# Kernel tuning notes

Hardware: AMD Instinct MI355X
Metric: run time of the kernel (lower is better)

Reference implementation:

```python
import jax, jax.numpy as jnp
import numpy as np

T, D, E, I, TOP_K = 4096, 2048, 8, 4096, 2

def setup_inputs() -> dict:
    key = jax.random.key(0)
    k1, k2, k3, k4, k5 = jax.random.split(key, 5)
    s = 0.02
    return {
        "hidden_states": jax.random.normal(k1, (T, D), jnp.float32),
        "wr": jax.random.normal(k2, (E, D), jnp.float32) * s,
        "w1": jax.random.normal(k3, (E, I, D), jnp.float32) * s,
        "v1": jax.random.normal(k4, (E, I, D), jnp.float32) * s,
        "w2": jax.random.normal(k5, (E, D, I), jnp.float32) * s,
        "index": 0,
    }

def reference(hidden_states, wr, w1, v1, w2, index):
    # index selects the layer; n_layers == 1 here so weights are already that layer's.
    x = hidden_states.reshape(-1, D)  # [T, D]
    # Router logits + softmax top-k with renormalization (fused_moe semantics)
    logits = x @ wr.T                                  # [T, E]
    probs = jax.nn.softmax(logits, axis=-1)
    topw, topi = jax.lax.top_k(probs, TOP_K)           # [T, K]
    topw = topw / jnp.sum(topw, axis=-1, keepdims=True)
    # Dense per-token gate matrix, zero for non-selected experts
    t_idx = jnp.arange(x.shape[0])[:, None]
    gates = jnp.zeros((x.shape[0], E), x.dtype).at[t_idx, topi].set(topw)  # [T, E]
    # SiLU-GLU experts: (silu(x w1^T) * (x v1^T)) w2^T, combined by gates
    out = jnp.zeros_like(x)
    for e in range(E):  # fixed small expert count
        h = jax.nn.silu(x @ w1[e].T) * (x @ v1[e].T)   # [T, I]
        out = out + gates[:, e:e + 1] * (h @ w2[e].T)  # [T, D]
    return out
```

## Files before the change

kernel.cpp:

```cpp
#include <hip/hip_runtime.h>
#include <hip/hip_bf16.h>
#include <cstdint>


#define T_TOK 4096
#define DHID  2048
#define NEXP  8
#define IDIM  4096
#define NSLOT (T_TOK * 2)

#define BM 128
#define BK 64

typedef __bf16 bf16x8 __attribute__((ext_vector_type(8)));
typedef __bf16 bf16x4 __attribute__((ext_vector_type(4)));
typedef float  f32x4  __attribute__((ext_vector_type(4)));

__device__ __forceinline__ void gload_lds16(const void* g, void* l) {
    __builtin_amdgcn_global_load_lds(
        (const __attribute__((address_space(1))) uint32_t*)g,
        (__attribute__((address_space(3))) uint32_t*)l, 16, 0, 0);
}

__global__ __launch_bounds__(256) void router_kernel(
    const float* __restrict__ x, const float* __restrict__ wr,
    __bf16* __restrict__ xb, int* __restrict__ topi, float* __restrict__ topg,
    int* __restrict__ cnt)
{
    int wave = threadIdx.x >> 6, lane = threadIdx.x & 63;
    int t = blockIdx.x * 4 + wave;
    const float4* xr = (const float4*)(x + (size_t)t * DHID);
    bf16x4* xbo = (bf16x4*)(xb + (size_t)t * DHID);
    float acc[NEXP];
#pragma unroll
    for (int e = 0; e < NEXP; ++e) acc[e] = 0.f;
#pragma unroll
    for (int j = 0; j < DHID / 256; ++j) {
        int d4 = lane + j * 64;
        float4 v = xr[d4];
        bf16x4 bv;
        bv[0] = (__bf16)v.x; bv[1] = (__bf16)v.y;
        bv[2] = (__bf16)v.z; bv[3] = (__bf16)v.w;
        xbo[d4] = bv;
#pragma unroll
        for (int e = 0; e < NEXP; ++e) {
            float4 w = ((const float4*)(wr + e * DHID))[d4];
            acc[e] += v.x * w.x + v.y * w.y + v.z * w.z + v.w * w.w;
        }
    }
#pragma unroll
    for (int e = 0; e < NEXP; ++e) {
#pragma unroll
        for (int s = 32; s > 0; s >>= 1) acc[e] += __shfl_xor(acc[e], s);
    }
    if (lane == 0) {
        int e0 = 0; float l0 = acc[0];
#pragma unroll
        for (int e = 1; e < NEXP; ++e) if (acc[e] > l0) { l0 = acc[e]; e0 = e; }
        int e1 = -1; float l1 = -3.4e38f;
#pragma unroll
        for (int e = 0; e < NEXP; ++e) if (e != e0 && acc[e] > l1) { l1 = acc[e]; e1 = e; }
        float g0 = 1.f / (1.f + __expf(l1 - l0));
        topi[t * 2] = e0; topi[t * 2 + 1] = e1;
        topg[t * 2] = g0; topg[t * 2 + 1] = 1.f - g0;
        atomicAdd(&cnt[e0], 1); atomicAdd(&cnt[e1], 1);
    }
}

__global__ void scan_kernel(const int* __restrict__ cnt, int* __restrict__ basep,
                            int* __restrict__ fill)
{
    if (threadIdx.x == 0 && blockIdx.x == 0) {
        int s = 0;
#pragma unroll
        for (int e = 0; e < NEXP; ++e) { basep[e] = s; s += cnt[e]; fill[e] = 0; }
    }
}

__global__ __launch_bounds__(256) void assign_kernel(
    const int* __restrict__ topi, const float* __restrict__ topg,
    const int* __restrict__ basep, int* __restrict__ fill,
    int* __restrict__ tok_of_slot, float* __restrict__ gate_of_slot,
    int* __restrict__ slot_of)
{
    int t = blockIdx.x * 256 + threadIdx.x;
    if (t >= T_TOK) return;
#pragma unroll
    for (int k = 0; k < 2; ++k) {
        int e = topi[t * 2 + k];
        int slot = basep[e] + atomicAdd(&fill[e], 1);
        tok_of_slot[slot] = t;
        gate_of_slot[slot] = topg[t * 2 + k];
        slot_of[t * 2 + k] = slot;
    }
}

__global__ __launch_bounds__(256) void convert2_kernel(
    const float* __restrict__ s1, __bf16* __restrict__ d1,
    const float* __restrict__ s2, __bf16* __restrict__ d2, size_t n8)
{
    for (size_t i = (size_t)blockIdx.x * 256 + threadIdx.x; i < n8;
         i += (size_t)gridDim.x * 256) {
        {
            const float4* s = (const float4*)(s1 + i * 8);
            float4 a = s[0], b = s[1];
            bf16x8 o;
            o[0]=(__bf16)a.x; o[1]=(__bf16)a.y; o[2]=(__bf16)a.z; o[3]=(__bf16)a.w;
            o[4]=(__bf16)b.x; o[5]=(__bf16)b.y; o[6]=(__bf16)b.z; o[7]=(__bf16)b.w;
            *(bf16x8*)(d1 + i * 8) = o;
        }
        if (s2) {
            const float4* s = (const float4*)(s2 + i * 8);
            float4 a = s[0], b = s[1];
            bf16x8 o;
            o[0]=(__bf16)a.x; o[1]=(__bf16)a.y; o[2]=(__bf16)a.z; o[3]=(__bf16)a.w;
            o[4]=(__bf16)b.x; o[5]=(__bf16)b.y; o[6]=(__bf16)b.z; o[7]=(__bf16)b.w;
            *(bf16x8*)(d2 + i * 8) = o;
        }
    }
}

template <int PASS, int KDIM>
__global__ __launch_bounds__(256, 2) void moe_gemm(
    const __bf16* __restrict__ Abase,
    const __bf16* __restrict__ Wa, const __bf16* __restrict__ Wb,
    const int* __restrict__ tok_of_slot, const float* __restrict__ gate_of_slot,
    const int* __restrict__ cnt, const int* __restrict__ basep,
    __bf16* __restrict__ Out, int e0)
{
    int ez = blockIdx.z;
    int eg = e0 + ez;
    int ne = cnt[eg];
    int m0 = blockIdx.y * BM;
    if (m0 >= ne) return;
    int n0 = blockIdx.x * (PASS == 1 ? 128 : 256);
    int sbase = basep[eg] + m0;

    __shared__ __bf16 As[BM * BK];
    __shared__ __bf16 B1s[BM * BK];
    __shared__ __bf16 B2s[BM * BK];
    __shared__ int   toks[BM];
    __shared__ float gates[BM];

    int tid = threadIdx.x, lane = tid & 63, wave = tid >> 6;
    char* AsB = (char*)&As[0];
    char* B1B = (char*)&B1s[0];
    char* B2B = (char*)&B2s[0];

    if (PASS == 1) {
        if (tid < BM) toks[tid] = (m0 + tid < ne) ? tok_of_slot[sbase + tid] : 0;
    } else {
        if (tid < BM) gates[tid] = gate_of_slot[(m0 + tid < ne) ? (sbase + tid) : sbase];
    }
    __syncthreads();

    const __bf16* a_src[4];
    int coff[4];
#pragma unroll
    for (int r = 0; r < 4; ++r) {
        int chunk = wave * 4 + r;
        int arow  = chunk * 8 + (lane >> 3);
        int csw   = (lane & 7) ^ (arow & 7);
        size_t rowbase;
        if (PASS == 1) {
            rowbase = (size_t)toks[arow] * KDIM;
        } else {
            int srow = (m0 + arow < ne) ? (sbase + arow) : sbase;
            rowbase = (size_t)srow * KDIM;
        }
        a_src[r] = Abase + rowbase + csw * 8;
        coff[r]  = chunk * 1024;
    }

    const __bf16* b1_src[4];
    const __bf16* b2_src[4];
    {
        const __bf16* Wae;
        const __bf16* Wbe;
        if (PASS == 1) {
            Wae = Wa + (size_t)ez * IDIM * DHID;
            Wbe = Wb + (size_t)ez * IDIM * DHID;
        } else {
            Wae = Wa + (size_t)ez * DHID * IDIM;
            Wbe = Wae + (size_t)128 * KDIM;
        }
#pragma unroll
        for (int r = 0; r < 4; ++r) {
            int chunk = wave * 4 + r;
            int brow  = chunk * 8 + (lane >> 3);
            int csw   = (lane & 7) ^ (brow & 7);
            b1_src[r] = Wae + (size_t)(n0 + brow) * KDIM + csw * 8;
            b2_src[r] = Wbe + (size_t)(n0 + brow) * KDIM + csw * 8;
        }
    }

    int wr0 = (wave >> 1) * 64, wc0 = (wave & 1) * 64;

    f32x4 acc1[4][4], acc2[4][4];
    f32x4 zf = {0.f, 0.f, 0.f, 0.f};
#pragma unroll
    for (int m = 0; m < 4; ++m)
#pragma unroll
        for (int n = 0; n < 4; ++n) { acc1[m][n] = zf; acc2[m][n] = zf; }

    const int NK = KDIM / BK;
    for (int t = 0; t < NK; ++t) {
        int ko = t * BK;
#pragma unroll
        for (int r = 0; r < 4; ++r) gload_lds16(a_src[r] + ko, AsB + coff[r]);
#pragma unroll
        for (int r = 0; r < 4; ++r) gload_lds16(b1_src[r] + ko, B1B + coff[r]);
#pragma unroll
        for (int r = 0; r < 4; ++r) gload_lds16(b2_src[r] + ko, B2B + coff[r]);
        __syncthreads();
#pragma unroll
        for (int ks = 0; ks < 2; ++ks) {
            int kb = ks * 64 + (lane >> 4) * 16;
            bf16x8 af[4], b1f[4], b2f[4];
#pragma unroll
            for (int m = 0; m < 4; ++m) {
                int row = wr0 + m * 16 + (lane & 15);
                af[m] = *(const bf16x8*)(AsB + row * 128 + (kb ^ ((row & 7) << 4)));
            }
#pragma unroll
            for (int n = 0; n < 4; ++n) {
                int row = wc0 + n * 16 + (lane & 15);
                int off = row * 128 + (kb ^ ((row & 7) << 4));
                b1f[n] = *(const bf16x8*)(B1B + off);
                b2f[n] = *(const bf16x8*)(B2B + off);
            }
#pragma unroll
            for (int m = 0; m < 4; ++m)
#pragma unroll
                for (int n = 0; n < 4; ++n) {
                    acc1[m][n] = __builtin_amdgcn_mfma_f32_16x16x32_bf16(af[m], b1f[n], acc1[m][n], 0, 0, 0);
                    acc2[m][n] = __builtin_amdgcn_mfma_f32_16x16x32_bf16(af[m], b2f[n], acc2[m][n], 0, 0, 0);
                }
        }
        __syncthreads();
    }

#pragma unroll
    for (int m = 0; m < 4; ++m) {
        int rbase = wr0 + m * 16 + ((lane >> 4) * 4);
#pragma unroll
        for (int n = 0; n < 4; ++n) {
            int col = wc0 + n * 16 + (lane & 15);
#pragma unroll
            for (int r = 0; r < 4; ++r) {
                int lrow = rbase + r;
                if (m0 + lrow < ne) {
                    if (PASS == 1) {
                        float a = acc1[m][n][r];
                        float b = acc2[m][n][r];
                        float h = (a / (1.f + __expf(-a))) * b;
                        Out[(size_t)(sbase + lrow) * IDIM + n0 + col] = (__bf16)h;
                    } else {
                        float g = gates[lrow];
                        size_t obase = (size_t)(sbase + lrow) * DHID + n0;
                        Out[obase + col]       = (__bf16)(acc1[m][n][r] * g);
                        Out[obase + 128 + col] = (__bf16)(acc2[m][n][r] * g);
                    }
                }
            }
        }
    }
}

__global__ __launch_bounds__(256) void combine_kernel(
    const __bf16* __restrict__ outslot, const int* __restrict__ slot_of,
    float* __restrict__ out)
{
    int idx = blockIdx.x * 256 + threadIdx.x;
    int t = idx >> 8;
    int c = (idx & 255) * 8;
    int s0 = slot_of[t * 2], s1 = slot_of[t * 2 + 1];
    bf16x8 a = *(const bf16x8*)(outslot + (size_t)s0 * DHID + c);
    bf16x8 b = *(const bf16x8*)(outslot + (size_t)s1 * DHID + c);
    float4 o0, o1;
    o0.x = (float)a[0] + (float)b[0];
    o0.y = (float)a[1] + (float)b[1];
    o0.z = (float)a[2] + (float)b[2];
    o0.w = (float)a[3] + (float)b[3];
    o1.x = (float)a[4] + (float)b[4];
    o1.y = (float)a[5] + (float)b[5];
    o1.z = (float)a[6] + (float)b[6];
    o1.w = (float)a[7] + (float)b[7];
    *(float4*)(out + (size_t)t * DHID + c)     = o0;
    *(float4*)(out + (size_t)t * DHID + c + 4) = o1;
}

extern "C" void kernel_launch(void* const* d_in, const int* in_sizes, int n_in,
                              void* d_out, int out_size, void* d_ws, size_t ws_size,
                              hipStream_t stream)
{
    (void)in_sizes; (void)n_in; (void)out_size; (void)ws_size;
    const float* x  = (const float*)d_in[0];
    const float* wr = (const float*)d_in[1];
    const float* w1 = (const float*)d_in[2];
    const float* v1 = (const float*)d_in[3];
    const float* w2 = (const float*)d_in[4];
    float* out = (float*)d_out;

    char* ws = (char*)d_ws;
    size_t off = 0;
    auto alloc = [&](size_t bytes) -> void* {
        void* p = ws + off;
        off += bytes;
        off = (off + 255) & ~(size_t)255;
        return p;
    };
    __bf16* xb      = (__bf16*)alloc((size_t)T_TOK * DHID * 2);
    __bf16* H       = (__bf16*)alloc((size_t)NSLOT * IDIM * 2);
    __bf16* outslot = (__bf16*)alloc((size_t)NSLOT * DHID * 2);
    int*    topi    = (int*)  alloc((size_t)T_TOK * 2 * 4);
    float*  topg    = (float*)alloc((size_t)T_TOK * 2 * 4);
    int*    tok_of_slot  = (int*)  alloc((size_t)NSLOT * 4);
    float*  gate_of_slot = (float*)alloc((size_t)NSLOT * 4);
    int*    slot_of = (int*)  alloc((size_t)NSLOT * 4);
    int*    cnt     = (int*)  alloc(NEXP * 4);
    int*    basep   = (int*)  alloc(NEXP * 4);
    int*    fill    = (int*)  alloc(NEXP * 4);

    const size_t EW = (size_t)IDIM * DHID;
    __bf16* chunkbuf = (__bf16*)alloc(4 * EW * 2);
    __bf16* pb1 = chunkbuf;
    __bf16* pb2 = chunkbuf + 2 * EW;
    __bf16* db  = chunkbuf;

    hipMemsetAsync(cnt, 0, NEXP * 4, stream);
    router_kernel<<<T_TOK / 4, 256, 0, stream>>>(x, wr, xb, topi, topg, cnt);
    scan_kernel<<<1, 64, 0, stream>>>(cnt, basep, fill);
    assign_kernel<<<T_TOK / 256, 256, 0, stream>>>(topi, topg, basep, fill,
                                                   tok_of_slot, gate_of_slot, slot_of);

    for (int c = 0; c < 4; ++c) {
        int e0 = c * 2;
        convert2_kernel<<<2048, 256, 0, stream>>>(
            w1 + (size_t)e0 * EW, pb1, v1 + (size_t)e0 * EW, pb2, (2 * EW) / 8);
        moe_gemm<1, DHID><<<dim3(IDIM / 128, NSLOT / BM, 2), 256, 0, stream>>>(
            xb, pb1, pb2, tok_of_slot, gate_of_slot, cnt, basep, H, e0);
    }
    for (int c = 0; c < 2; ++c) {
        int e0 = c * 4;
        convert2_kernel<<<2048, 256, 0, stream>>>(
            w2 + (size_t)e0 * EW, db, nullptr, nullptr, (4 * EW) / 8);
        moe_gemm<2, IDIM><<<dim3(DHID / 256, NSLOT / BM, 4), 256, 0, stream>>>(
            H, db, nullptr, tok_of_slot, gate_of_slot, cnt, basep, outslot, e0);
    }
    combine_kernel<<<(T_TOK * DHID / 8) / 256, 256, 0, stream>>>(outslot, slot_of, out);
}
```

Baseline: 978.3 us.

## Convert all expert weights upfront and overlap conversion with router and GEMM

Replaces the chunked per-expert-pair convert-then-GEMM loop with a full-size bf16 weight buffer. w1/v1 conversion is folded into the router launch as extra blocks, and w2 conversion runs as an extra z-slice of the first GEMM grid when workspace allows. Each GEMM pass then runs as one launch over all 8 experts. This removes launch serialization and the small per-chunk grids, at the cost of much more workspace and conversion blocks that compete with the GEMM for bandwidth and CUs.

```diff
diff --git a/kernel.cpp b/kernel.cpp
--- a/kernel.cpp
+++ b/kernel.cpp
@@ -22,11 +22,33 @@
         (__attribute__((address_space(3))) uint32_t*)l, 16, 0, 0);
 }
 
-__global__ __launch_bounds__(256) void router_kernel(
+__device__ __forceinline__ void cvt8(const float* __restrict__ s, __bf16* __restrict__ d,
+                                     size_t i) {
+    const float4* sp = (const float4*)(s + i * 8);
+    float4 a = sp[0], b = sp[1];
+    bf16x8 o;
+    o[0]=(__bf16)a.x; o[1]=(__bf16)a.y; o[2]=(__bf16)a.z; o[3]=(__bf16)a.w;
+    o[4]=(__bf16)b.x; o[5]=(__bf16)b.y; o[6]=(__bf16)b.z; o[7]=(__bf16)b.w;
+    *(bf16x8*)(d + i * 8) = o;
+}
+
+__global__ __launch_bounds__(256) void router_cvt_kernel(
     const float* __restrict__ x, const float* __restrict__ wr,
     __bf16* __restrict__ xb, int* __restrict__ topi, float* __restrict__ topg,
-    int* __restrict__ cnt)
-{
+    int* __restrict__ cnt,
+    const float* __restrict__ w1, __bf16* __restrict__ wb1,
+    const float* __restrict__ v1, __bf16* __restrict__ wv1, size_t n8)
+{
+    if (blockIdx.x >= T_TOK / 4) {
+        size_t cb = blockIdx.x - T_TOK / 4;
+        size_t gid = cb * 256 + threadIdx.x;
+        size_t stride = (size_t)(gridDim.x - T_TOK / 4) * 256;
+        for (size_t i = gid; i < n8; i += stride) {
+            cvt8(w1, wb1, i);
+            cvt8(v1, wv1, i);
+        }
+        return;
+    }
     int wave = threadIdx.x >> 6, lane = threadIdx.x & 63;
     int t = blockIdx.x * 4 + wave;
     const float4* xr = (const float4*)(x + (size_t)t * DHID);
@@ -95,29 +117,11 @@
     }
 }
 
-__global__ __launch_bounds__(256) void convert2_kernel(
-    const float* __restrict__ s1, __bf16* __restrict__ d1,
-    const float* __restrict__ s2, __bf16* __restrict__ d2, size_t n8)
+__global__ __launch_bounds__(256) void convert_kernel(
+    const float* __restrict__ src, __bf16* __restrict__ dst, size_t n8)
 {
     for (size_t i = (size_t)blockIdx.x * 256 + threadIdx.x; i < n8;
-         i += (size_t)gridDim.x * 256) {
-        {
-            const float4* s = (const float4*)(s1 + i * 8);
-            float4 a = s[0], b = s[1];
-            bf16x8 o;
-            o[0]=(__bf16)a.x; o[1]=(__bf16)a.y; o[2]=(__bf16)a.z; o[3]=(__bf16)a.w;
-            o[4]=(__bf16)b.x; o[5]=(__bf16)b.y; o[6]=(__bf16)b.z; o[7]=(__bf16)b.w;
-            *(bf16x8*)(d1 + i * 8) = o;
-        }
-        if (s2) {
-            const float4* s = (const float4*)(s2 + i * 8);
-            float4 a = s[0], b = s[1];
-            bf16x8 o;
-            o[0]=(__bf16)a.x; o[1]=(__bf16)a.y; o[2]=(__bf16)a.z; o[3]=(__bf16)a.w;
-            o[4]=(__bf16)b.x; o[5]=(__bf16)b.y; o[6]=(__bf16)b.z; o[7]=(__bf16)b.w;
-            *(bf16x8*)(d2 + i * 8) = o;
-        }
-    }
+         i += (size_t)gridDim.x * 256) cvt8(src, dst, i);
 }
 
 template <int PASS, int KDIM>
@@ -126,15 +130,21 @@
     const __bf16* __restrict__ Wa, const __bf16* __restrict__ Wb,
     const int* __restrict__ tok_of_slot, const float* __restrict__ gate_of_slot,
     const int* __restrict__ cnt, const int* __restrict__ basep,
-    __bf16* __restrict__ Out, int e0)
-{
-    int ez = blockIdx.z;
-    int eg = e0 + ez;
-    int ne = cnt[eg];
+    __bf16* __restrict__ Out,
+    const float* __restrict__ cvt_src, __bf16* __restrict__ cvt_dst, size_t cvt_n8)
+{
+    int e = blockIdx.z;
+    if (e >= NEXP) {
+        size_t gid = ((size_t)blockIdx.y * gridDim.x + blockIdx.x) * 256 + threadIdx.x;
+        size_t stride = (size_t)gridDim.x * gridDim.y * 256;
+        for (size_t i = gid; i < cvt_n8; i += stride) cvt8(cvt_src, cvt_dst, i);
+        return;
+    }
+    int ne = cnt[e];
     int m0 = blockIdx.y * BM;
     if (m0 >= ne) return;
     int n0 = blockIdx.x * (PASS == 1 ? 128 : 256);
-    int sbase = basep[eg] + m0;
+    int sbase = basep[e] + m0;
 
     __shared__ __bf16 As[BM * BK];
     __shared__ __bf16 B1s[BM * BK];
@@ -178,10 +188,10 @@
         const __bf16* Wae;
         const __bf16* Wbe;
         if (PASS == 1) {
-            Wae = Wa + (size_t)ez * IDIM * DHID;
-            Wbe = Wb + (size_t)ez * IDIM * DHID;
+            Wae = Wa + (size_t)e * IDIM * DHID;
+            Wbe = Wb + (size_t)e * IDIM * DHID;
         } else {
-            Wae = Wa + (size_t)ez * DHID * IDIM;
+            Wae = Wa + (size_t)e * DHID * IDIM;
             Wbe = Wae + (size_t)128 * KDIM;
         }
 #pragma unroll
@@ -294,7 +304,7 @@
                               void* d_out, int out_size, void* d_ws, size_t ws_size,
                               hipStream_t stream)
 {
-    (void)in_sizes; (void)n_in; (void)out_size; (void)ws_size;
+    (void)in_sizes; (void)n_in; (void)out_size;
     const float* x  = (const float*)d_in[0];
     const float* wr = (const float*)d_in[1];
     const float* w1 = (const float*)d_in[2];
@@ -322,31 +332,29 @@
     int*    basep   = (int*)  alloc(NEXP * 4);
     int*    fill    = (int*)  alloc(NEXP * 4);
 
-    const size_t EW = (size_t)IDIM * DHID;
-    __bf16* chunkbuf = (__bf16*)alloc(4 * EW * 2);
-    __bf16* pb1 = chunkbuf;
-    __bf16* pb2 = chunkbuf + 2 * EW;
-    __bf16* db  = chunkbuf;
+    const size_t EW   = (size_t)IDIM * DHID;
+    const size_t WALL = (size_t)NEXP * EW;
+    __bf16* wb1 = (__bf16*)alloc(WALL * 2);
+    __bf16* wv1 = (__bf16*)alloc(WALL * 2);
+    bool roomy = (ws_size >= off + WALL * 2 + (16u << 20));
+    __bf16* wb2 = roomy ? (__bf16*)alloc(WALL * 2) : wb1;
 
     hipMemsetAsync(cnt, 0, NEXP * 4, stream);
-    router_kernel<<<T_TOK / 4, 256, 0, stream>>>(x, wr, xb, topi, topg, cnt);
+    router_cvt_kernel<<<T_TOK / 4 + 4096, 256, 0, stream>>>(
+        x, wr, xb, topi, topg, cnt, w1, wb1, v1, wv1, WALL / 8);
     scan_kernel<<<1, 64, 0, stream>>>(cnt, basep, fill);
     assign_kernel<<<T_TOK / 256, 256, 0, stream>>>(topi, topg, basep, fill,
                                                    tok_of_slot, gate_of_slot, slot_of);
-
-    for (int c = 0; c < 4; ++c) {
-        int e0 = c * 2;
-        convert2_kernel<<<2048, 256, 0, stream>>>(
-            w1 + (size_t)e0 * EW, pb1, v1 + (size_t)e0 * EW, pb2, (2 * EW) / 8);
-        moe_gemm<1, DHID><<<dim3(IDIM / 128, NSLOT / BM, 2), 256, 0, stream>>>(
-            xb, pb1, pb2, tok_of_slot, gate_of_slot, cnt, basep, H, e0);
-    }
-    for (int c = 0; c < 2; ++c) {
-        int e0 = c * 4;
-        convert2_kernel<<<2048, 256, 0, stream>>>(
-            w2 + (size_t)e0 * EW, db, nullptr, nullptr, (4 * EW) / 8);
-        moe_gemm<2, IDIM><<<dim3(DHID / 256, NSLOT / BM, 4), 256, 0, stream>>>(
-            H, db, nullptr, tok_of_slot, gate_of_slot, cnt, basep, outslot, e0);
-    }
+    if (roomy) {
+        moe_gemm<1, DHID><<<dim3(IDIM / 128, NSLOT / BM, NEXP + 1), 256, 0, stream>>>(
+            xb, wb1, wv1, tok_of_slot, gate_of_slot, cnt, basep, H, w2, wb2, WALL / 8);
+    } else {
+        moe_gemm<1, DHID><<<dim3(IDIM / 128, NSLOT / BM, NEXP), 256, 0, stream>>>(
+            xb, wb1, wv1, tok_of_slot, gate_of_slot, cnt, basep, H, nullptr, nullptr, 0);
+        convert_kernel<<<2048, 256, 0, stream>>>(w2, wb2, WALL / 8);
+    }
+    moe_gemm<2, IDIM><<<dim3(DHID / 256, NSLOT / BM, NEXP), 256, 0, stream>>>(
+        H, wb2, nullptr, tok_of_slot, gate_of_slot, cnt, basep, outslot,
+        nullptr, nullptr, 0);
     combine_kernel<<<(T_TOK * DHID / 8) / 256, 256, 0, stream>>>(outslot, slot_of, out);
 }
```

Result: faster. 842.0 us (median of 2 runs) (-13.9%).

## Fuse fp32-to-bf16 weight conversion into MoE GEMM tile loads

Applied to the files above, without the earlier changes.

Removes the separate convert kernels that wrote bf16 copies of the expert weights and instead streams fp32 weights straight into LDS, converting to bf16 when fragments are read. All experts now run in a single launch per pass instead of chunked launches. This drops the extra write and re-read of the converted weights and the launch serialization, but doubles weight bytes per tile and LDS footprint. It also adds conversion ALU work in the inner loop, and the larger LDS use may reduce occupancy.

```diff
diff --git a/kernel.cpp b/kernel.cpp
--- a/kernel.cpp
+++ b/kernel.cpp
@@ -20,6 +20,15 @@
     __builtin_amdgcn_global_load_lds(
         (const __attribute__((address_space(1))) uint32_t*)g,
         (__attribute__((address_space(3))) uint32_t*)l, 16, 0, 0);
+}
+
+__device__ __forceinline__ bf16x8 ldcvt8(const char* p) {
+    float4 lo = *(const float4*)(p);
+    float4 hi = *(const float4*)(p + 16);
+    bf16x8 o;
+    o[0]=(__bf16)lo.x; o[1]=(__bf16)lo.y; o[2]=(__bf16)lo.z; o[3]=(__bf16)lo.w;
+    o[4]=(__bf16)hi.x; o[5]=(__bf16)hi.y; o[6]=(__bf16)hi.z; o[7]=(__bf16)hi.w;
+    return o;
 }
 
 __global__ __launch_bounds__(256) void router_kernel(
@@ -95,67 +104,32 @@
     }
 }
 
-__global__ __launch_bounds__(256) void convert2_kernel(
-    const float* __restrict__ s1, __bf16* __restrict__ d1,
-    const float* __restrict__ s2, __bf16* __restrict__ d2, size_t n8)
-{
-    for (size_t i = (size_t)blockIdx.x * 256 + threadIdx.x; i < n8;
-         i += (size_t)gridDim.x * 256) {
-        {
-            const float4* s = (const float4*)(s1 + i * 8);
-            float4 a = s[0], b = s[1];
-            bf16x8 o;
-            o[0]=(__bf16)a.x; o[1]=(__bf16)a.y; o[2]=(__bf16)a.z; o[3]=(__bf16)a.w;
-            o[4]=(__bf16)b.x; o[5]=(__bf16)b.y; o[6]=(__bf16)b.z; o[7]=(__bf16)b.w;
-            *(bf16x8*)(d1 + i * 8) = o;
-        }
-        if (s2) {
-            const float4* s = (const float4*)(s2 + i * 8);
-            float4 a = s[0], b = s[1];
-            bf16x8 o;
-            o[0]=(__bf16)a.x; o[1]=(__bf16)a.y; o[2]=(__bf16)a.z; o[3]=(__bf16)a.w;
-            o[4]=(__bf16)b.x; o[5]=(__bf16)b.y; o[6]=(__bf16)b.z; o[7]=(__bf16)b.w;
-            *(bf16x8*)(d2 + i * 8) = o;
-        }
-    }
-}
-
 template <int PASS, int KDIM>
 __global__ __launch_bounds__(256, 2) void moe_gemm(
     const __bf16* __restrict__ Abase,
-    const __bf16* __restrict__ Wa, const __bf16* __restrict__ Wb,
+    const float* __restrict__ Wa, const float* __restrict__ Wb,
     const int* __restrict__ tok_of_slot, const float* __restrict__ gate_of_slot,
     const int* __restrict__ cnt, const int* __restrict__ basep,
-    __bf16* __restrict__ Out, int e0)
-{
-    int ez = blockIdx.z;
-    int eg = e0 + ez;
-    int ne = cnt[eg];
+    __bf16* __restrict__ Out)
+{
+    int e  = blockIdx.z;
+    int ne = cnt[e];
     int m0 = blockIdx.y * BM;
     if (m0 >= ne) return;
     int n0 = blockIdx.x * (PASS == 1 ? 128 : 256);
-    int sbase = basep[eg] + m0;
+    int sbase = basep[e] + m0;
 
     __shared__ __bf16 As[BM * BK];
-    __shared__ __bf16 B1s[BM * BK];
-    __shared__ __bf16 B2s[BM * BK];
-    __shared__ int   toks[BM];
-    __shared__ float gates[BM];
+    __shared__ float  B1s[128 * BK];
+    __shared__ float  B2s[128 * BK];
 
     int tid = threadIdx.x, lane = tid & 63, wave = tid >> 6;
     char* AsB = (char*)&As[0];
     char* B1B = (char*)&B1s[0];
     char* B2B = (char*)&B2s[0];
 
-    if (PASS == 1) {
-        if (tid < BM) toks[tid] = (m0 + tid < ne) ? tok_of_slot[sbase + tid] : 0;
-    } else {
-        if (tid < BM) gates[tid] = gate_of_slot[(m0 + tid < ne) ? (sbase + tid) : sbase];
-    }
-    __syncthreads();
-
     const __bf16* a_src[4];
-    int coff[4];
+    int a_coff[4];
 #pragma unroll
     for (int r = 0; r < 4; ++r) {
         int chunk = wave * 4 + r;
@@ -163,34 +137,39 @@
         int csw   = (lane & 7) ^ (arow & 7);
         size_t rowbase;
         if (PASS == 1) {
-            rowbase = (size_t)toks[arow] * KDIM;
+            int tok = (m0 + arow < ne) ? tok_of_slot[sbase + arow] : 0;
+            rowbase = (size_t)tok * KDIM;
         } else {
             int srow = (m0 + arow < ne) ? (sbase + arow) : sbase;
             rowbase = (size_t)srow * KDIM;
         }
-        a_src[r] = Abase + rowbase + csw * 8;
-        coff[r]  = chunk * 1024;
-    }
-
-    const __bf16* b1_src[4];
-    const __bf16* b2_src[4];
+        a_src[r]  = Abase + rowbase + csw * 8;
+        a_coff[r] = chunk * 1024;
+    }
+
+    const float* b1_src[8];
+    int b_coff[8];
+    ptrdiff_t bdelta;
     {
-        const __bf16* Wae;
-        const __bf16* Wbe;
+        const float* Wae;
+        const float* Wbe;
         if (PASS == 1) {
-            Wae = Wa + (size_t)ez * IDIM * DHID;
-            Wbe = Wb + (size_t)ez * IDIM * DHID;
+            Wae = Wa + (size_t)e * IDIM * DHID;
+            Wbe = Wb + (size_t)e * IDIM * DHID;
         } else {
-            Wae = Wa + (size_t)ez * DHID * IDIM;
+            Wae = Wa + (size_t)e * DHID * IDIM;
             Wbe = Wae + (size_t)128 * KDIM;
         }
-#pragma unroll
-        for (int r = 0; r < 4; ++r) {
-            int chunk = wave * 4 + r;
-            int brow  = chunk * 8 + (lane >> 3);
-            int csw   = (lane & 7) ^ (brow & 7);
-            b1_src[r] = Wae + (size_t)(n0 + brow) * KDIM + csw * 8;
-            b2_src[r] = Wbe + (size_t)(n0 + brow) * KDIM + csw * 8;
+        bdelta = (const char*)Wbe - (const char*)Wae;
+#pragma unroll
+        for (int r = 0; r < 8; ++r) {
+            int chunk = wave * 8 + r;
+            int brow  = chunk * 4 + (lane >> 4);
+            int u     = lane & 15;
+            int slot  = u >> 1, half = u & 1;
+            int elem  = ((slot ^ (brow & 7)) * 8 + half * 4);
+            b1_src[r] = Wae + (size_t)(n0 + brow) * KDIM + elem;
+            b_coff[r] = chunk * 1024;
         }
     }
 
@@ -207,15 +186,17 @@
     for (int t = 0; t < NK; ++t) {
         int ko = t * BK;
 #pragma unroll
-        for (int r = 0; r < 4; ++r) gload_lds16(a_src[r] + ko, AsB + coff[r]);
-#pragma unroll
-        for (int r = 0; r < 4; ++r) gload_lds16(b1_src[r] + ko, B1B + coff[r]);
-#pragma unroll
-        for (int r = 0; r < 4; ++r) gload_lds16(b2_src[r] + ko, B2B + coff[r]);
+        for (int r = 0; r < 4; ++r) gload_lds16(a_src[r] + ko, AsB + a_coff[r]);
+#pragma unroll
+        for (int r = 0; r < 8; ++r) gload_lds16(b1_src[r] + ko, B1B + b_coff[r]);
+#pragma unroll
+        for (int r = 0; r < 8; ++r)
+            gload_lds16((const char*)(b1_src[r] + ko) + bdelta, B2B + b_coff[r]);
         __syncthreads();
 #pragma unroll
         for (int ks = 0; ks < 2; ++ks) {
             int kb = ks * 64 + (lane >> 4) * 16;
+            int bslot = ks * 4 + (lane >> 4);
             bf16x8 af[4], b1f[4], b2f[4];
 #pragma unroll
             for (int m = 0; m < 4; ++m) {
@@ -225,9 +206,9 @@
 #pragma unroll
             for (int n = 0; n < 4; ++n) {
                 int row = wc0 + n * 16 + (lane & 15);
-                int off = row * 128 + (kb ^ ((row & 7) << 4));
-                b1f[n] = *(const bf16x8*)(B1B + off);
-                b2f[n] = *(const bf16x8*)(B2B + off);
+                int off = row * 256 + ((bslot ^ (row & 7)) << 5);
+                b1f[n] = ldcvt8(B1B + off);
+                b2f[n] = ldcvt8(B2B + off);
             }
 #pragma unroll
             for (int m = 0; m < 4; ++m)
@@ -256,7 +237,7 @@
                         float h = (a / (1.f + __expf(-a))) * b;
                         Out[(size_t)(sbase + lrow) * IDIM + n0 + col] = (__bf16)h;
                     } else {
-                        float g = gates[lrow];
+                        float g = gate_of_slot[sbase + lrow];
                         size_t obase = (size_t)(sbase + lrow) * DHID + n0;
                         Out[obase + col]       = (__bf16)(acc1[m][n][r] * g);
                         Out[obase + 128 + col] = (__bf16)(acc2[m][n][r] * g);
@@ -322,31 +303,14 @@
     int*    basep   = (int*)  alloc(NEXP * 4);
     int*    fill    = (int*)  alloc(NEXP * 4);
 
-    const size_t EW = (size_t)IDIM * DHID;
-    __bf16* chunkbuf = (__bf16*)alloc(4 * EW * 2);
-    __bf16* pb1 = chunkbuf;
-    __bf16* pb2 = chunkbuf + 2 * EW;
-    __bf16* db  = chunkbuf;
-
     hipMemsetAsync(cnt, 0, NEXP * 4, stream);
     router_kernel<<<T_TOK / 4, 256, 0, stream>>>(x, wr, xb, topi, topg, cnt);
     scan_kernel<<<1, 64, 0, stream>>>(cnt, basep, fill);
     assign_kernel<<<T_TOK / 256, 256, 0, stream>>>(topi, topg, basep, fill,
                                                    tok_of_slot, gate_of_slot, slot_of);
-
-    for (int c = 0; c < 4; ++c) {
-        int e0 = c * 2;
-        convert2_kernel<<<2048, 256, 0, stream>>>(
-            w1 + (size_t)e0 * EW, pb1, v1 + (size_t)e0 * EW, pb2, (2 * EW) / 8);
-        moe_gemm<1, DHID><<<dim3(IDIM / 128, NSLOT / BM, 2), 256, 0, stream>>>(
-            xb, pb1, pb2, tok_of_slot, gate_of_slot, cnt, basep, H, e0);
-    }
-    for (int c = 0; c < 2; ++c) {
-        int e0 = c * 4;
-        convert2_kernel<<<2048, 256, 0, stream>>>(
-            w2 + (size_t)e0 * EW, db, nullptr, nullptr, (4 * EW) / 8);
-        moe_gemm<2, IDIM><<<dim3(DHID / 256, NSLOT / BM, 4), 256, 0, stream>>>(
-            H, db, nullptr, tok_of_slot, gate_of_slot, cnt, basep, outslot, e0);
-    }
+    moe_gemm<1, DHID><<<dim3(IDIM / 128, NSLOT / BM, NEXP), 256, 0, stream>>>(
+        xb, w1, v1, tok_of_slot, gate_of_slot, cnt, basep, H);
+    moe_gemm<2, IDIM><<<dim3(DHID / 256, NSLOT / BM, NEXP), 256, 0, stream>>>(
+        H, w2, nullptr, tok_of_slot, gate_of_slot, cnt, basep, outslot);
     combine_kernel<<<(T_TOK * DHID / 8) / 256, 256, 0, stream>>>(outslot, slot_of, out);
 }
```

New measurement: 1.992 ms. 104% more time.
